# Optimization experiments

Hardware: AMD Instinct MI355X
Metric: run time of the kernel (lower is better)

Reference implementation:

```python
import jax, jax.numpy as jnp
import numpy as np

T, B, I, H = 512, 64, 256, 256
ACT_EXP2 = 7   # activation scale = 2^-7
W_EXP2 = 8     # weight scale = 2^-8
QMIN, QMAX = -128.0, 127.0  # int8 symmetric, zp=0


def fq(x, exp2_inv):
    """Fake-quantize (round/clamp/dequant) with straight-through estimator."""
    scale = 2.0 ** (-exp2_inv)
    y = jnp.clip(jnp.round(x / scale), QMIN, QMAX) * scale
    return x + jax.lax.stop_gradient(y - x)


def setup_inputs() -> dict:
    key = jax.random.key(0)
    k = jax.random.split(key, 5)
    x = jax.random.normal(k[0], (T, B, I), jnp.float32)
    h0 = jnp.zeros((B, H), jnp.float32)
    W = jax.random.normal(k[1], (I, 3 * H), jnp.float32) / np.sqrt(I)
    R = jax.random.normal(k[2], (H, 3 * H), jnp.float32) / np.sqrt(H)
    bx = jax.random.normal(k[3], (3 * H,), jnp.float32) * 0.1
    br = jax.random.normal(k[4], (3 * H,), jnp.float32) * 0.1
    return {"x": x, "h0": h0, "W": W, "R": R, "bx": bx, "br": br}


def gru_quant(x, h0, W, R, bx, br):
    # quantize weights/biases once (weight.W / weight.R / weight.bx / weight.br)
    Wq = fq(W, W_EXP2)
    Rq = fq(R, W_EXP2)
    bxq = fq(bx, W_EXP2)
    brq = fq(br, W_EXP2)
    # hoisted input matmul: Wx = fq(fq(x) @ Wq)  -> [T, B, 3H]
    Wx = fq(jnp.einsum('tbi,ij->tbj', fq(x, ACT_EXP2), Wq), ACT_EXP2)
    Hh = h0.shape[-1]
    bz, brg, bg = bxq[:Hh], bxq[Hh:2 * Hh], bxq[2 * Hh:]

    def step(h, wx_t):
        hq = fq(h, ACT_EXP2)                      # input.h
        Rh = fq(hq @ Rq, ACT_EXP2)                # matmul.Rh
        v = fq(Rh + brq, ACT_EXP2)                # op.Rh_add_br
        wz, wr, wg = wx_t[:, :Hh], wx_t[:, Hh:2 * Hh], wx_t[:, 2 * Hh:]
        vz, vr, vg = v[:, :Hh], v[:, Hh:2 * Hh], v[:, 2 * Hh:]
        z = fq(jax.nn.sigmoid(fq(wz + bz + vz, ACT_EXP2)), ACT_EXP2)  # gate.z
        r = fq(jax.nn.sigmoid(fq(wr + brg + vr, ACT_EXP2)), ACT_EXP2)  # gate.r
        rRh = fq(r * vg, ACT_EXP2)                # op.rRh
        g = fq(jnp.tanh(fq(wg + bg + rRh, ACT_EXP2)), ACT_EXP2)        # gate.g
        old = fq(z * h, ACT_EXP2)                 # op.old_contrib
        new = fq((1.0 - z) * g, ACT_EXP2)         # op.new_contrib
        h_new = old + new
        return h_new, h_new

    _, hs = jax.lax.scan(step, h0, Wx)  # hs: [T, B, H]
    return hs


def reference(x, h0, W, R, bx, br):
    return gru_quant(x, h0, W, R, bx, br)
```

## Files before the change

### kernel.cpp

```cpp
#include <hip/hip_runtime.h>
#include <hip/hip_bf16.h>
#include <stdint.h>


#define T_STEPS 512
#define BATCH   64
#define IDIM    256
#define HDIM    256
#define N3H     768

#if defined(__has_builtin)
#if __has_builtin(__builtin_amdgcn_sdot4)
#define DOT4(a,b,c) __builtin_amdgcn_sdot4((int)(a),(int)(b),(int)(c),false)
#endif
#endif
#ifndef DOT4
__device__ __forceinline__ int dot4_sw(uint32_t a, uint32_t b, int c){
  c += (int)(int8_t)(a)      * (int)(int8_t)(b);
  c += (int)(int8_t)(a>>8)   * (int)(int8_t)(b>>8);
  c += (int)(int8_t)(a>>16)  * (int)(int8_t)(b>>16);
  c += (int)(int8_t)(a>>24)  * (int)(int8_t)(b>>24);
  return c;
}
#define DOT4(a,b,c) dot4_sw((uint32_t)(a),(uint32_t)(b),(int)(c))
#endif

#define CHUNK(W,c) (((c)&3)==0 ? W[(c)>>2].x : ((c)&3)==1 ? W[(c)>>2].y : \
                    ((c)&3)==2 ? W[(c)>>2].z : W[(c)>>2].w)

__device__ __forceinline__ void barrier_lds() {
  asm volatile("s_waitcnt lgkmcnt(0)\n\ts_barrier" ::: "memory");
}

__device__ __forceinline__ int clamp8(int x)   { return min(127, max(-128, x)); }
__device__ __forceinline__ int rne_half(int y) { int t = y >> 1; return t + (t & y & 1); }
__device__ __forceinline__ int rne_s8(int s)   { return (s + 127 + ((s >> 8) & 1)) >> 8; }
__device__ __forceinline__ int rne_s7(int p)   { return (p + 63 + ((p >> 7) & 1)) >> 7; }

__device__ __forceinline__ int rneclamp(float v) {
  int q = (int)rintf(v);
  return min(127, max(-128, q));
}

__device__ __forceinline__ uint32_t packq4(float4 f, float sc) {
  uint32_t b0 = (uint32_t)(uint8_t)(int8_t)rneclamp(f.x * sc);
  uint32_t b1 = (uint32_t)(uint8_t)(int8_t)rneclamp(f.y * sc);
  uint32_t b2 = (uint32_t)(uint8_t)(int8_t)rneclamp(f.z * sc);
  uint32_t b3 = (uint32_t)(uint8_t)(int8_t)rneclamp(f.w * sc);
  return b0 | (b1 << 8) | (b2 << 16) | (b3 << 24);
}

__global__ void prep_kernel(const float* __restrict__ W, const float* __restrict__ R,
                            const float* __restrict__ bx, const float* __restrict__ br,
                            int8_t* __restrict__ Wq, int8_t* __restrict__ Rq,
                            int8_t* __restrict__ bx8, int8_t* __restrict__ br8) {
  const int NW = IDIM * N3H;
  int idx = blockIdx.x * 256 + threadIdx.x;
  if (idx < NW) {
    int k = idx / N3H, j = idx % N3H;
    Wq[((size_t)(k >> 4) * N3H + j) * 16 + (k & 15)] = (int8_t)rneclamp(W[idx] * 256.0f);
  } else if (idx < 2 * NW) {
    int i2 = idx - NW;
    int k = i2 / N3H, j = i2 % N3H;
    Rq[(size_t)j * HDIM + k] = (int8_t)rneclamp(R[i2] * 256.0f);
  } else if (idx < 2 * NW + N3H) {
    int i2 = idx - 2 * NW;
    bx8[i2] = (int8_t)rneclamp(bx[i2] * 256.0f);
  } else if (idx < 2 * NW + 2 * N3H) {
    int i2 = idx - 2 * NW - N3H;
    br8[i2] = (int8_t)rneclamp(br[i2] * 256.0f);
  }
}

__global__ __launch_bounds__(768, 1) void gemm_wx_kernel(
    const float* __restrict__ x, const int8_t* __restrict__ Wq,
    int8_t* __restrict__ WxQ8) {
  const int t = blockIdx.x;
  const int j = threadIdx.x;

  __shared__ uint4 xq4[64 * 16];
  uint32_t* xq = (uint32_t*)xq4;

  uint4 w[16];
  const uint4* wp = (const uint4*)Wq;
  #pragma unroll
  for (int kk = 0; kk < 16; ++kk) w[kk] = wp[kk * N3H + j];

  const float4* xg = (const float4*)(x) + (size_t)t * 4096;
  for (int i = j; i < 4096; i += 768) {
    float4 f = xg[i];
    xq[i] = packq4(f, 128.0f);
  }
  __syncthreads();

  for (int r = 0; r < 64; ++r) {
    int s = 0;
    #pragma unroll
    for (int kk = 0; kk < 16; ++kk) {
      uint4 hv = xq4[r * 16 + kk];
      s = DOT4(hv.x, w[kk].x, s);
      s = DOT4(hv.y, w[kk].y, s);
      s = DOT4(hv.z, w[kk].z, s);
      s = DOT4(hv.w, w[kk].w, s);
    }
    int q = clamp8(rne_s8(s));
    WxQ8[((size_t)r * T_STEPS + t) * N3H + j] = (int8_t)q;
  }
}

__global__ __launch_bounds__(256, 1) __attribute__((amdgpu_waves_per_eu(1, 1)))
void gru_rec6_kernel(
    const float* __restrict__ h0, const int8_t* __restrict__ Rq,
    const int8_t* __restrict__ bx8, const int8_t* __restrict__ br8,
    const int8_t* __restrict__ WxQ8, float* __restrict__ out) {
  const int b = blockIdx.x;
  const int j = threadIdx.x;
  const int lane = j & 63;

  __shared__ uint32_t hq[2][64];
  __shared__ int8_t lutS[256];
  __shared__ int8_t lutT[256];

  uint4 wz[16], wr[16], wg[16];
  {
    const uint4* pz = (const uint4*)(Rq + (size_t)j * HDIM);
    const uint4* pr = (const uint4*)(Rq + (size_t)(j + 256) * HDIM);
    const uint4* pg = (const uint4*)(Rq + (size_t)(j + 512) * HDIM);
    #pragma unroll
    for (int kk = 0; kk < 16; ++kk) { wz[kk] = pz[kk]; wr[kk] = pr[kk]; wg[kk] = pg[kk]; }
  }
  const int bz  = (int)bx8[j];
  const int brg = (int)bx8[j + 256];
  const int bg  = (int)bx8[j + 512];
  const int vbz = (int)br8[j];
  const int vbr = (int)br8[j + 256];
  const int vbg = (int)br8[j + 512];

  {
    double a = ((double)j - 128.0) / 128.0;
    lutS[j] = (int8_t)min(127, max(-128, (int)rint(128.0 / (1.0 + exp(-a)))));
    lutT[j] = (int8_t)min(127, max(-128, (int)rint(128.0 * tanh(a))));
  }
  int hi = (int)rintf(h0[b * HDIM + j] * 128.0f);
  ((int8_t*)&hq[0][0])[j] = (int8_t)clamp8(hi);
  __syncthreads();

  const int8_t* wxp = WxQ8 + (size_t)b * T_STEPS * N3H + j;
  float* outp = out + (size_t)b * HDIM + j;

  int wxA0 = (int)wxp[0],   wxA1 = (int)wxp[256],       wxA2 = (int)wxp[512];
  int wxB0 = (int)wxp[N3H], wxB1 = (int)wxp[N3H + 256], wxB2 = (int)wxp[N3H + 512];

  for (int t = 0; t < T_STEPS; ++t) {
    const int cur = t & 1, nxt = cur ^ 1;

    const int8_t* p = wxp + (size_t)min(t + 2, T_STEPS - 1) * N3H;
    int nz = (int)p[0], nr = (int)p[256], ng = (int)p[512];

    uint32_t hw = hq[cur][lane];
    int sz = 0, sr = 0, sg = 0;
    #pragma unroll
    for (int c = 0; c < 64; ++c) {
      int hc = __builtin_amdgcn_readlane((int)hw, c);
      sz = DOT4(hc, CHUNK(wz, c), sz);
      sr = DOT4(hc, CHUNK(wr, c), sr);
      sg = DOT4(hc, CHUNK(wg, c), sg);
    }
    int vz = clamp8(rne_half(2 * clamp8(rne_s8(sz)) + vbz));
    int vr = clamp8(rne_half(2 * clamp8(rne_s8(sr)) + vbr));
    int vg = clamp8(rne_half(2 * clamp8(rne_s8(sg)) + vbg));

    int az = clamp8(rne_half(2 * (wxA0 + vz) + bz));
    int zi = (int)lutS[az + 128];
    int ar = clamp8(rne_half(2 * (wxA1 + vr) + brg));
    int ri = (int)lutS[ar + 128];
    int rrh = clamp8(rne_s7(ri * vg));
    int ag = clamp8(rne_half(2 * (wxA2 + rrh) + bg));
    int gi = (int)lutT[ag + 128];
    int oldi = clamp8(rne_s7(zi * hi));
    int newi = clamp8(rne_s7((128 - zi) * gi));
    hi = oldi + newi;
    outp[(size_t)t * BATCH * HDIM] = (float)hi * (1.0f / 128.0f);
    ((int8_t*)&hq[nxt][0])[j] = (int8_t)clamp8(hi);

    wxA0 = wxB0; wxA1 = wxB1; wxA2 = wxB2;
    wxB0 = nz;   wxB1 = nr;   wxB2 = ng;

    barrier_lds();
  }
}

extern "C" void kernel_launch(void* const* d_in, const int* in_sizes, int n_in,
                              void* d_out, int out_size, void* d_ws, size_t ws_size,
                              hipStream_t stream) {
  const float* x  = (const float*)d_in[0];
  const float* h0 = (const float*)d_in[1];
  const float* W  = (const float*)d_in[2];
  const float* R  = (const float*)d_in[3];
  const float* bx = (const float*)d_in[4];
  const float* br = (const float*)d_in[5];
  float* out = (float*)d_out;

  const size_t NW = (size_t)IDIM * N3H;
  int8_t* Wq  = (int8_t*)d_ws;
  int8_t* Rq  = Wq + NW;
  int8_t* bx8 = Rq + NW;
  int8_t* br8 = bx8 + N3H;
  int8_t* WxQ8 = br8 + N3H;

  {
    int total = (int)(2 * NW + 2 * N3H);
    int blocks = (total + 255) / 256;
    prep_kernel<<<blocks, 256, 0, stream>>>(W, R, bx, br, Wq, Rq, bx8, br8);
  }
  gemm_wx_kernel<<<T_STEPS, 768, 0, stream>>>(x, Wq, WxQ8);
  gru_rec6_kernel<<<BATCH, 256, 0, stream>>>(h0, Rq, bx8, br8, WxQ8, out);
}
```

Before: 473.9 us.

## Process two batch rows per block in GRU recurrence to interleave dot chains

The recurrent kernel now handles two batch elements per 256-thread block, sharing the register-resident Rq weights across both. The two independent dot-product and gate chains are interleaved so each step has more parallel work to hide readlane and dot latency. The grid halves to 32 blocks, and each thread's per-step instruction count roughly doubles, which may lengthen the serial step if issue-bound.

New measurement: 807.7 us. +70.4%, slower.

```diff
diff --git a/kernel.cpp b/kernel.cpp
--- a/kernel.cpp
+++ b/kernel.cpp
@@ -108,16 +108,18 @@
   }
 }
 
-__global__ __launch_bounds__(256, 1) __attribute__((amdgpu_waves_per_eu(1, 1)))
-void gru_rec6_kernel(
+__global__ __launch_bounds__(256, 1)
+void gru_rec8_kernel(
     const float* __restrict__ h0, const int8_t* __restrict__ Rq,
     const int8_t* __restrict__ bx8, const int8_t* __restrict__ br8,
     const int8_t* __restrict__ WxQ8, float* __restrict__ out) {
-  const int b = blockIdx.x;
+  const int bA = blockIdx.x * 2;
+  const int bB = bA + 1;
   const int j = threadIdx.x;
   const int lane = j & 63;
 
-  __shared__ uint32_t hq[2][64];
+  __shared__ uint32_t hqA[2][64];
+  __shared__ uint32_t hqB[2][64];
   __shared__ int8_t lutS[256];
   __shared__ int8_t lutT[256];
 
@@ -141,50 +143,83 @@
     lutS[j] = (int8_t)min(127, max(-128, (int)rint(128.0 / (1.0 + exp(-a)))));
     lutT[j] = (int8_t)min(127, max(-128, (int)rint(128.0 * tanh(a))));
   }
-  int hi = (int)rintf(h0[b * HDIM + j] * 128.0f);
-  ((int8_t*)&hq[0][0])[j] = (int8_t)clamp8(hi);
+  int hiA = (int)rintf(h0[bA * HDIM + j] * 128.0f);
+  int hiB = (int)rintf(h0[bB * HDIM + j] * 128.0f);
+  ((int8_t*)&hqA[0][0])[j] = (int8_t)clamp8(hiA);
+  ((int8_t*)&hqB[0][0])[j] = (int8_t)clamp8(hiB);
   __syncthreads();
 
-  const int8_t* wxp = WxQ8 + (size_t)b * T_STEPS * N3H + j;
-  float* outp = out + (size_t)b * HDIM + j;
-
-  int wxA0 = (int)wxp[0],   wxA1 = (int)wxp[256],       wxA2 = (int)wxp[512];
-  int wxB0 = (int)wxp[N3H], wxB1 = (int)wxp[N3H + 256], wxB2 = (int)wxp[N3H + 512];
+  const int8_t* wxpA = WxQ8 + (size_t)bA * T_STEPS * N3H + j;
+  const int8_t* wxpB = WxQ8 + (size_t)bB * T_STEPS * N3H + j;
+  float* outpA = out + (size_t)bA * HDIM + j;
+  float* outpB = out + (size_t)bB * HDIM + j;
+
+  int wxA0 = (int)wxpA[0],   wxA1 = (int)wxpA[256],       wxA2 = (int)wxpA[512];
+  int wxA0n = (int)wxpA[N3H], wxA1n = (int)wxpA[N3H + 256], wxA2n = (int)wxpA[N3H + 512];
+  int wxB0 = (int)wxpB[0],   wxB1 = (int)wxpB[256],       wxB2 = (int)wxpB[512];
+  int wxB0n = (int)wxpB[N3H], wxB1n = (int)wxpB[N3H + 256], wxB2n = (int)wxpB[N3H + 512];
 
   for (int t = 0; t < T_STEPS; ++t) {
     const int cur = t & 1, nxt = cur ^ 1;
 
-    const int8_t* p = wxp + (size_t)min(t + 2, T_STEPS - 1) * N3H;
-    int nz = (int)p[0], nr = (int)p[256], ng = (int)p[512];
-
-    uint32_t hw = hq[cur][lane];
-    int sz = 0, sr = 0, sg = 0;
+    const int8_t* pA = wxpA + (size_t)min(t + 2, T_STEPS - 1) * N3H;
+    const int8_t* pB = wxpB + (size_t)min(t + 2, T_STEPS - 1) * N3H;
+    int nzA = (int)pA[0], nrA = (int)pA[256], ngA = (int)pA[512];
+    int nzB = (int)pB[0], nrB = (int)pB[256], ngB = (int)pB[512];
+
+    uint32_t hwA = hqA[cur][lane];
+    uint32_t hwB = hqB[cur][lane];
+    int szA = 0, srA = 0, sgA = 0, szB = 0, srB = 0, sgB = 0;
     #pragma unroll
     for (int c = 0; c < 64; ++c) {
-      int hc = __builtin_amdgcn_readlane((int)hw, c);
-      sz = DOT4(hc, CHUNK(wz, c), sz);
-      sr = DOT4(hc, CHUNK(wr, c), sr);
-      sg = DOT4(hc, CHUNK(wg, c), sg);
-    }
-    int vz = clamp8(rne_half(2 * clamp8(rne_s8(sz)) + vbz));
-    int vr = clamp8(rne_half(2 * clamp8(rne_s8(sr)) + vbr));
-    int vg = clamp8(rne_half(2 * clamp8(rne_s8(sg)) + vbg));
-
-    int az = clamp8(rne_half(2 * (wxA0 + vz) + bz));
-    int zi = (int)lutS[az + 128];
-    int ar = clamp8(rne_half(2 * (wxA1 + vr) + brg));
-    int ri = (int)lutS[ar + 128];
-    int rrh = clamp8(rne_s7(ri * vg));
-    int ag = clamp8(rne_half(2 * (wxA2 + rrh) + bg));
-    int gi = (int)lutT[ag + 128];
-    int oldi = clamp8(rne_s7(zi * hi));
-    int newi = clamp8(rne_s7((128 - zi) * gi));
-    hi = oldi + newi;
-    outp[(size_t)t * BATCH * HDIM] = (float)hi * (1.0f / 128.0f);
-    ((int8_t*)&hq[nxt][0])[j] = (int8_t)clamp8(hi);
-
-    wxA0 = wxB0; wxA1 = wxB1; wxA2 = wxB2;
-    wxB0 = nz;   wxB1 = nr;   wxB2 = ng;
+      int ha = __builtin_amdgcn_readlane((int)hwA, c);
+      int hb = __builtin_amdgcn_readlane((int)hwB, c);
+      szA = DOT4(ha, CHUNK(wz, c), szA);
+      szB = DOT4(hb, CHUNK(wz, c), szB);
+      srA = DOT4(ha, CHUNK(wr, c), srA);
+      srB = DOT4(hb, CHUNK(wr, c), srB);
+      sgA = DOT4(ha, CHUNK(wg, c), sgA);
+      sgB = DOT4(hb, CHUNK(wg, c), sgB);
+    }
+
+    {
+      int vz = clamp8(rne_half(2 * clamp8(rne_s8(szA)) + vbz));
+      int vr = clamp8(rne_half(2 * clamp8(rne_s8(srA)) + vbr));
+      int vg = clamp8(rne_half(2 * clamp8(rne_s8(sgA)) + vbg));
+      int az = clamp8(rne_half(2 * (wxA0 + vz) + bz));
+      int zi = (int)lutS[az + 128];
+      int ar = clamp8(rne_half(2 * (wxA1 + vr) + brg));
+      int ri = (int)lutS[ar + 128];
+      int rrh = clamp8(rne_s7(ri * vg));
+      int ag = clamp8(rne_half(2 * (wxA2 + rrh) + bg));
+      int gi = (int)lutT[ag + 128];
+      int oldi = clamp8(rne_s7(zi * hiA));
+      int newi = clamp8(rne_s7((128 - zi) * gi));
+      hiA = oldi + newi;
+      outpA[(size_t)t * BATCH * HDIM] = (float)hiA * (1.0f / 128.0f);
+      ((int8_t*)&hqA[nxt][0])[j] = (int8_t)clamp8(hiA);
+      wxA0 = wxA0n; wxA1 = wxA1n; wxA2 = wxA2n;
+      wxA0n = nzA;  wxA1n = nrA;  wxA2n = ngA;
+    }
+    {
+      int vz = clamp8(rne_half(2 * clamp8(rne_s8(szB)) + vbz));
+      int vr = clamp8(rne_half(2 * clamp8(rne_s8(srB)) + vbr));
+      int vg = clamp8(rne_half(2 * clamp8(rne_s8(sgB)) + vbg));
+      int az = clamp8(rne_half(2 * (wxB0 + vz) + bz));
+      int zi = (int)lutS[az + 128];
+      int ar = clamp8(rne_half(2 * (wxB1 + vr) + brg));
+      int ri = (int)lutS[ar + 128];
+      int rrh = clamp8(rne_s7(ri * vg));
+      int ag = clamp8(rne_half(2 * (wxB2 + rrh) + bg));
+      int gi = (int)lutT[ag + 128];
+      int oldi = clamp8(rne_s7(zi * hiB));
+      int newi = clamp8(rne_s7((128 - zi) * gi));
+      hiB = oldi + newi;
+      outpB[(size_t)t * BATCH * HDIM] = (float)hiB * (1.0f / 128.0f);
+      ((int8_t*)&hqB[nxt][0])[j] = (int8_t)clamp8(hiB);
+      wxB0 = wxB0n; wxB1 = wxB1n; wxB2 = wxB2n;
+      wxB0n = nzB;  wxB1n = nrB;  wxB2n = ngB;
+    }
 
     barrier_lds();
   }
@@ -214,5 +249,5 @@
     prep_kernel<<<blocks, 256, 0, stream>>>(W, R, bx, br, Wq, Rq, bx8, br8);
   }
   gemm_wx_kernel<<<T_STEPS, 768, 0, stream>>>(x, Wq, WxQ8);
-  gru_rec6_kernel<<<BATCH, 256, 0, stream>>>(h0, Rq, bx8, br8, WxQ8, out);
-}
+  gru_rec8_kernel<<<BATCH / 2, 256, 0, stream>>>(h0, Rq, bx8, br8, WxQ8, out);
+}
```

## Split GRU recurrence across two wave groups: z/r gates and g gate

Applied to the files above, without the earlier changes.

The recurrent kernel now launches 512 threads per batch row instead of 256. The first 256 threads compute the z and r gate dot products and pass them through shared memory. The other 256 compute the g dot product and then finish the hidden-state update. This cuts the serial per-thread dot-product chain per step from three gates to at most two, and lowers register pressure per thread. In exchange each timestep needs two barriers instead of one and an extra shared-memory handoff.

New measurement: 556.4 us. +17.4%, slower.

```diff
diff --git a/kernel.cpp b/kernel.cpp
--- a/kernel.cpp
+++ b/kernel.cpp
@@ -108,85 +108,122 @@
   }
 }
 
-__global__ __launch_bounds__(256, 1) __attribute__((amdgpu_waves_per_eu(1, 1)))
-void gru_rec6_kernel(
+__global__ __launch_bounds__(512) __attribute__((amdgpu_waves_per_eu(2, 2)))
+void gru_rec10_kernel(
     const float* __restrict__ h0, const int8_t* __restrict__ Rq,
     const int8_t* __restrict__ bx8, const int8_t* __restrict__ br8,
     const int8_t* __restrict__ WxQ8, float* __restrict__ out) {
   const int b = blockIdx.x;
-  const int j = threadIdx.x;
-  const int lane = j & 63;
+  const int tid = threadIdx.x;
+  const int j = tid & 255;
+  const int lane = tid & 63;
 
   __shared__ uint32_t hq[2][64];
+  __shared__ int zirl[256];
   __shared__ int8_t lutS[256];
   __shared__ int8_t lutT[256];
 
-  uint4 wz[16], wr[16], wg[16];
-  {
-    const uint4* pz = (const uint4*)(Rq + (size_t)j * HDIM);
-    const uint4* pr = (const uint4*)(Rq + (size_t)(j + 256) * HDIM);
-    const uint4* pg = (const uint4*)(Rq + (size_t)(j + 512) * HDIM);
-    #pragma unroll
-    for (int kk = 0; kk < 16; ++kk) { wz[kk] = pz[kk]; wr[kk] = pr[kk]; wg[kk] = pg[kk]; }
-  }
-  const int bz  = (int)bx8[j];
-  const int brg = (int)bx8[j + 256];
-  const int bg  = (int)bx8[j + 512];
-  const int vbz = (int)br8[j];
-  const int vbr = (int)br8[j + 256];
-  const int vbg = (int)br8[j + 512];
-
   {
     double a = ((double)j - 128.0) / 128.0;
-    lutS[j] = (int8_t)min(127, max(-128, (int)rint(128.0 / (1.0 + exp(-a)))));
-    lutT[j] = (int8_t)min(127, max(-128, (int)rint(128.0 * tanh(a))));
-  }
-  int hi = (int)rintf(h0[b * HDIM + j] * 128.0f);
-  ((int8_t*)&hq[0][0])[j] = (int8_t)clamp8(hi);
+    if (tid < 256) {
+      lutS[j] = (int8_t)min(127, max(-128, (int)rint(128.0 / (1.0 + exp(-a)))));
+    } else {
+      lutT[j] = (int8_t)min(127, max(-128, (int)rint(128.0 * tanh(a))));
+      int h00 = (int)rintf(h0[b * HDIM + j] * 128.0f);
+      ((int8_t*)&hq[0][0])[j] = (int8_t)clamp8(h00);
+    }
+  }
   __syncthreads();
 
-  const int8_t* wxp = WxQ8 + (size_t)b * T_STEPS * N3H + j;
-  float* outp = out + (size_t)b * HDIM + j;
-
-  int wxA0 = (int)wxp[0],   wxA1 = (int)wxp[256],       wxA2 = (int)wxp[512];
-  int wxB0 = (int)wxp[N3H], wxB1 = (int)wxp[N3H + 256], wxB2 = (int)wxp[N3H + 512];
-
-  for (int t = 0; t < T_STEPS; ++t) {
-    const int cur = t & 1, nxt = cur ^ 1;
-
-    const int8_t* p = wxp + (size_t)min(t + 2, T_STEPS - 1) * N3H;
-    int nz = (int)p[0], nr = (int)p[256], ng = (int)p[512];
-
-    uint32_t hw = hq[cur][lane];
-    int sz = 0, sr = 0, sg = 0;
-    #pragma unroll
-    for (int c = 0; c < 64; ++c) {
-      int hc = __builtin_amdgcn_readlane((int)hw, c);
-      sz = DOT4(hc, CHUNK(wz, c), sz);
-      sr = DOT4(hc, CHUNK(wr, c), sr);
-      sg = DOT4(hc, CHUNK(wg, c), sg);
-    }
-    int vz = clamp8(rne_half(2 * clamp8(rne_s8(sz)) + vbz));
-    int vr = clamp8(rne_half(2 * clamp8(rne_s8(sr)) + vbr));
-    int vg = clamp8(rne_half(2 * clamp8(rne_s8(sg)) + vbg));
-
-    int az = clamp8(rne_half(2 * (wxA0 + vz) + bz));
-    int zi = (int)lutS[az + 128];
-    int ar = clamp8(rne_half(2 * (wxA1 + vr) + brg));
-    int ri = (int)lutS[ar + 128];
-    int rrh = clamp8(rne_s7(ri * vg));
-    int ag = clamp8(rne_half(2 * (wxA2 + rrh) + bg));
-    int gi = (int)lutT[ag + 128];
-    int oldi = clamp8(rne_s7(zi * hi));
-    int newi = clamp8(rne_s7((128 - zi) * gi));
-    hi = oldi + newi;
-    outp[(size_t)t * BATCH * HDIM] = (float)hi * (1.0f / 128.0f);
-    ((int8_t*)&hq[nxt][0])[j] = (int8_t)clamp8(hi);
-
-    wxA0 = wxB0; wxA1 = wxB1; wxA2 = wxB2;
-    wxB0 = nz;   wxB1 = nr;   wxB2 = ng;
-
-    barrier_lds();
+  if (tid < 256) {
+    uint4 wz[16], wr[16];
+    {
+      const uint4* pz = (const uint4*)(Rq + (size_t)j * HDIM);
+      const uint4* pr = (const uint4*)(Rq + (size_t)(j + 256) * HDIM);
+      #pragma unroll
+      for (int kk = 0; kk < 16; ++kk) { wz[kk] = pz[kk]; wr[kk] = pr[kk]; }
+    }
+    const int bz  = (int)bx8[j];
+    const int brg = (int)bx8[j + 256];
+    const int vbz = (int)br8[j];
+    const int vbr = (int)br8[j + 256];
+    const int8_t* wxp = WxQ8 + (size_t)b * T_STEPS * N3H + j;
+
+    int zA = (int)wxp[0],   rA = (int)wxp[256];
+    int zB = (int)wxp[N3H], rB = (int)wxp[N3H + 256];
+
+    for (int t = 0; t < T_STEPS; ++t) {
+      const int cur = t & 1;
+      const int8_t* p = wxp + (size_t)min(t + 2, T_STEPS - 1) * N3H;
+      int zn = (int)p[0], rn = (int)p[256];
+
+      uint32_t hw = hq[cur][lane];
+      int sz = 0, sr = 0;
+      #pragma unroll
+      for (int c = 0; c < 64; ++c) {
+        int hc = __builtin_amdgcn_readlane((int)hw, c);
+        sz = DOT4(hc, CHUNK(wz, c), sz);
+        sr = DOT4(hc, CHUNK(wr, c), sr);
+      }
+      int vz = clamp8(rne_half(2 * clamp8(rne_s8(sz)) + vbz));
+      int vr = clamp8(rne_half(2 * clamp8(rne_s8(sr)) + vbr));
+      int az = clamp8(rne_half(2 * (zA + vz) + bz));
+      int zi = (int)lutS[az + 128];
+      int ar = clamp8(rne_half(2 * (rA + vr) + brg));
+      int ri = (int)lutS[ar + 128];
+      zirl[j] = zi | (ri << 16);
+
+      zA = zB; rA = rB; zB = zn; rB = rn;
+
+      barrier_lds();
+      barrier_lds();
+    }
+  } else {
+    uint4 wg[16];
+    {
+      const uint4* pg = (const uint4*)(Rq + (size_t)(j + 512) * HDIM);
+      #pragma unroll
+      for (int kk = 0; kk < 16; ++kk) wg[kk] = pg[kk];
+    }
+    const int bg  = (int)bx8[j + 512];
+    const int vbg = (int)br8[j + 512];
+    int hi = (int)rintf(h0[b * HDIM + j] * 128.0f);
+    const int8_t* wxp = WxQ8 + (size_t)b * T_STEPS * N3H + j + 512;
+    float* outp = out + (size_t)b * HDIM + j;
+
+    int gA = (int)wxp[0], gB = (int)wxp[N3H];
+
+    for (int t = 0; t < T_STEPS; ++t) {
+      const int cur = t & 1, nxt = cur ^ 1;
+      const int8_t* p = wxp + (size_t)min(t + 2, T_STEPS - 1) * N3H;
+      int gn = (int)p[0];
+
+      uint32_t hw = hq[cur][lane];
+      int sg = 0;
+      #pragma unroll
+      for (int c = 0; c < 64; ++c) {
+        int hc = __builtin_amdgcn_readlane((int)hw, c);
+        sg = DOT4(hc, CHUNK(wg, c), sg);
+      }
+      int vg = clamp8(rne_half(2 * clamp8(rne_s8(sg)) + vbg));
+
+      barrier_lds();
+      int zr_ = zirl[j];
+      int zi = zr_ & 0xffff;
+      int ri = zr_ >> 16;
+      int rrh = clamp8(rne_s7(ri * vg));
+      int ag = clamp8(rne_half(2 * (gA + rrh) + bg));
+      int gi = (int)lutT[ag + 128];
+      int oldi = clamp8(rne_s7(zi * hi));
+      int newi = clamp8(rne_s7((128 - zi) * gi));
+      hi = oldi + newi;
+      outp[(size_t)t * BATCH * HDIM] = (float)hi * (1.0f / 128.0f);
+      ((int8_t*)&hq[nxt][0])[j] = (int8_t)clamp8(hi);
+
+      gA = gB; gB = gn;
+
+      barrier_lds();
+    }
   }
 }
 
@@ -214,5 +251,5 @@
     prep_kernel<<<blocks, 256, 0, stream>>>(W, R, bx, br, Wq, Rq, bx8, br8);
   }
   gemm_wx_kernel<<<T_STEPS, 768, 0, stream>>>(x, Wq, WxQ8);
-  gru_rec6_kernel<<<BATCH, 256, 0, stream>>>(h0, Rq, bx8, br8, WxQ8, out);
-}
+  gru_rec10_kernel<<<BATCH, 512, 0, stream>>>(h0, Rq, bx8, br8, WxQ8, out);
+}
```

## Fold gate rounding into wide LUTs and read hidden state via LDS vectors

Applied to the files above, without the earlier changes.

Replaces the per-step readlane broadcast of the hidden state with uint4 LDS loads that every lane reads at the same address. Folds the rounding and clamping before the sigmoid and tanh into 2048-entry lookup tables. Replaces the r*vg multiply-and-round with a 64KB 2D table indexed by (ar, vg). This shortens the serial per-step dependency chain but adds about 70KB of dynamic LDS, a heavier table-building prologue, and drops the waves_per_eu attribute.

Result: faster. 460.0 us (-2.9%).

```diff
diff --git a/kernel.cpp b/kernel.cpp
--- a/kernel.cpp
+++ b/kernel.cpp
@@ -24,9 +24,6 @@
 }
 #define DOT4(a,b,c) dot4_sw((uint32_t)(a),(uint32_t)(b),(int)(c))
 #endif
-
-#define CHUNK(W,c) (((c)&3)==0 ? W[(c)>>2].x : ((c)&3)==1 ? W[(c)>>2].y : \
-                    ((c)&3)==2 ? W[(c)>>2].z : W[(c)>>2].w)
 
 __device__ __forceinline__ void barrier_lds() {
   asm volatile("s_waitcnt lgkmcnt(0)\n\ts_barrier" ::: "memory");
@@ -108,18 +105,19 @@
   }
 }
 
-__global__ __launch_bounds__(256, 1) __attribute__((amdgpu_waves_per_eu(1, 1)))
-void gru_rec6_kernel(
+__global__ __launch_bounds__(256, 1)
+void gru_rec12_kernel(
     const float* __restrict__ h0, const int8_t* __restrict__ Rq,
     const int8_t* __restrict__ bx8, const int8_t* __restrict__ br8,
     const int8_t* __restrict__ WxQ8, float* __restrict__ out) {
   const int b = blockIdx.x;
   const int j = threadIdx.x;
-  const int lane = j & 63;
-
-  __shared__ uint32_t hq[2][64];
-  __shared__ int8_t lutS[256];
-  __shared__ int8_t lutT[256];
+
+  extern __shared__ int8_t smem[];
+  int8_t*  lutRR = smem;
+  int8_t*  lutS2 = smem + 65536;
+  int8_t*  lutT2 = smem + 67584;
+  uint4*   hqb   = (uint4*)(smem + 69632);
 
   uint4 wz[16], wr[16], wg[16];
   {
@@ -129,20 +127,37 @@
     #pragma unroll
     for (int kk = 0; kk < 16; ++kk) { wz[kk] = pz[kk]; wr[kk] = pr[kk]; wg[kk] = pg[kk]; }
   }
-  const int bz  = (int)bx8[j];
-  const int brg = (int)bx8[j + 256];
-  const int bg  = (int)bx8[j + 512];
+  const int bzc = (int)bx8[j];
+  const int brc = (int)bx8[j + 256];
+  const int bgc = (int)bx8[j + 512];
   const int vbz = (int)br8[j];
   const int vbr = (int)br8[j + 256];
   const int vbg = (int)br8[j + 512];
 
   {
-    double a = ((double)j - 128.0) / 128.0;
-    lutS[j] = (int8_t)min(127, max(-128, (int)rint(128.0 / (1.0 + exp(-a)))));
-    lutT[j] = (int8_t)min(127, max(-128, (int)rint(128.0 * tanh(a))));
+    const double inv128 = 1.0 / 128.0;
+    #pragma unroll
+    for (int i = 0; i < 8; ++i) {
+      int y = j * 8 + i - 1024;
+      int v = clamp8(rne_half(y));
+      lutS2[j * 8 + i] = (int8_t)clamp8((int)rint(128.0 / (1.0 + exp(-(double)v * inv128))));
+      lutT2[j * 8 + i] = (int8_t)clamp8((int)rint(128.0 * tanh((double)v * inv128)));
+    }
+    int ri = clamp8((int)rint(128.0 / (1.0 + exp(-((double)j - 128.0) * inv128))));
+    uint32_t* rrw = (uint32_t*)lutRR;
+    for (int v4 = 0; v4 < 64; ++v4) {
+      uint32_t w = 0;
+      #pragma unroll
+      for (int e = 0; e < 4; ++e) {
+        int v = v4 * 4 + e - 128;
+        int rr = clamp8(rne_s7(ri * v));
+        w |= ((uint32_t)(uint8_t)(int8_t)rr) << (8 * e);
+      }
+      rrw[j * 64 + v4] = w;
+    }
   }
   int hi = (int)rintf(h0[b * HDIM + j] * 128.0f);
-  ((int8_t*)&hq[0][0])[j] = (int8_t)clamp8(hi);
+  ((int8_t*)&hqb[0])[j] = (int8_t)clamp8(hi);
   __syncthreads();
 
   const int8_t* wxp = WxQ8 + (size_t)b * T_STEPS * N3H + j;
@@ -157,31 +172,37 @@
     const int8_t* p = wxp + (size_t)min(t + 2, T_STEPS - 1) * N3H;
     int nz = (int)p[0], nr = (int)p[256], ng = (int)p[512];
 
-    uint32_t hw = hq[cur][lane];
+    const uint4* hc = &hqb[cur * 16];
     int sz = 0, sr = 0, sg = 0;
     #pragma unroll
-    for (int c = 0; c < 64; ++c) {
-      int hc = __builtin_amdgcn_readlane((int)hw, c);
-      sz = DOT4(hc, CHUNK(wz, c), sz);
-      sr = DOT4(hc, CHUNK(wr, c), sr);
-      sg = DOT4(hc, CHUNK(wg, c), sg);
+    for (int kk = 0; kk < 16; ++kk) {
+      uint4 hv = hc[kk];
+      sz = DOT4(hv.x, wz[kk].x, sz);
+      sr = DOT4(hv.x, wr[kk].x, sr);
+      sg = DOT4(hv.x, wg[kk].x, sg);
+      sz = DOT4(hv.y, wz[kk].y, sz);
+      sr = DOT4(hv.y, wr[kk].y, sr);
+      sg = DOT4(hv.y, wg[kk].y, sg);
+      sz = DOT4(hv.z, wz[kk].z, sz);
+      sr = DOT4(hv.z, wr[kk].z, sr);
+      sg = DOT4(hv.z, wg[kk].z, sg);
+      sz = DOT4(hv.w, wz[kk].w, sz);
+      sr = DOT4(hv.w, wr[kk].w, sr);
+      sg = DOT4(hv.w, wg[kk].w, sg);
     }
     int vz = clamp8(rne_half(2 * clamp8(rne_s8(sz)) + vbz));
     int vr = clamp8(rne_half(2 * clamp8(rne_s8(sr)) + vbr));
     int vg = clamp8(rne_half(2 * clamp8(rne_s8(sg)) + vbg));
 
-    int az = clamp8(rne_half(2 * (wxA0 + vz) + bz));
-    int zi = (int)lutS[az + 128];
-    int ar = clamp8(rne_half(2 * (wxA1 + vr) + brg));
-    int ri = (int)lutS[ar + 128];
-    int rrh = clamp8(rne_s7(ri * vg));
-    int ag = clamp8(rne_half(2 * (wxA2 + rrh) + bg));
-    int gi = (int)lutT[ag + 128];
+    int zi  = (int)lutS2[2 * (wxA0 + vz) + bzc + 1024];
+    int ar  = clamp8(rne_half(2 * (wxA1 + vr) + brc));
+    int rrh = (int)lutRR[((ar + 128) << 8) | (vg + 128)];
+    int gi  = (int)lutT2[2 * (wxA2 + rrh) + bgc + 1024];
     int oldi = clamp8(rne_s7(zi * hi));
     int newi = clamp8(rne_s7((128 - zi) * gi));
     hi = oldi + newi;
     outp[(size_t)t * BATCH * HDIM] = (float)hi * (1.0f / 128.0f);
-    ((int8_t*)&hq[nxt][0])[j] = (int8_t)clamp8(hi);
+    ((int8_t*)&hqb[nxt * 16])[j] = (int8_t)clamp8(hi);
 
     wxA0 = wxB0; wxA1 = wxB1; wxA2 = wxB2;
     wxB0 = nz;   wxB1 = nr;   wxB2 = ng;
@@ -214,5 +235,5 @@
     prep_kernel<<<blocks, 256, 0, stream>>>(W, R, bx, br, Wq, Rq, bx8, br8);
   }
   gemm_wx_kernel<<<T_STEPS, 768, 0, stream>>>(x, Wq, WxQ8);
-  gru_rec6_kernel<<<BATCH, 256, 0, stream>>>(h0, Rq, bx8, br8, WxQ8, out);
-}
+  gru_rec12_kernel<<<BATCH, 256, 70144, stream>>>(h0, Rq, bx8, br8, WxQ8, out);
+}
```
